# Kernel optimization log

Hardware: AMD Instinct MI355X
Metric: run time of the kernel (lower is better)

Reference implementation:

```python
import jax, jax.numpy as jnp
import numpy as np

B, N = 16384, 20
F = 128          # n_node_features = n_neighbors_features = embed_dim
T = 100          # time_dim
E = 128          # n_edge_features
H = 2            # n_head
OUT = 128        # output_dimension
KEY_DIM = F + T + E  # 356


def setup_inputs() -> dict:
    key = jax.random.key(0)
    ks = jax.random.split(key, 24)
    s = 0.02
    inp = {
        "src_node_features": jax.random.normal(ks[0], (B, F), jnp.float32),
        "neighbors_features": jax.random.normal(ks[1], (B, N, F), jnp.float32),
        "neighbors_time_features": jax.random.normal(ks[2], (B, N, T), jnp.float32),
        "edge_features": jax.random.normal(ks[3], (B, N, E), jnp.float32),
        "neighbors_padding_mask": jax.random.randint(ks[4], (B, N), 0, 2).astype(bool),
        "weights": jax.random.uniform(ks[5], (B, N), jnp.float32),
        # transform: Linear(key_dim -> F)
        "Wt": jax.random.normal(ks[6], (F, KEY_DIM), jnp.float32) * s,
        "bt": jnp.zeros((F,), jnp.float32),
        # MultiheadAttention projections (embed_dim = kdim = vdim = F)
        "Wq": jax.random.normal(ks[7], (F, F), jnp.float32) * s,
        "bq": jnp.zeros((F,), jnp.float32),
        "Wk": jax.random.normal(ks[8], (F, F), jnp.float32) * s,
        "bk": jnp.zeros((F,), jnp.float32),
        "Wv": jax.random.normal(ks[9], (F, F), jnp.float32) * s,
        "bv": jnp.zeros((F,), jnp.float32),
        "Wo": jax.random.normal(ks[10], (F, F), jnp.float32) * s,
        "bo": jnp.zeros((F,), jnp.float32),
        # MergeLayer: fc1(query_dim + F -> F), fc2(F -> OUT)
        "W1": jax.random.normal(ks[11], (F, F + F), jnp.float32) * s,
        "b1": jnp.zeros((F,), jnp.float32),
        "W2": jax.random.normal(ks[12], (OUT, F), jnp.float32) * s,
        "b2": jnp.zeros((OUT,), jnp.float32),
    }
    return inp


def _gat_forward(src, nbr, timef, edgef, w, mask,
                 Wt, bt, Wq, bq, Wk, bk, Wv, bv, Wo, bo, W1, b1, W2, b2):
    b, f = src.shape
    dh = f // H
    scale = 1.0 / jnp.sqrt(jnp.asarray(dh, src.dtype))
    # key = transform(cat([nbr, edge, time])) * weights  -> [B,N,F]
    k_in = jnp.concatenate([nbr, edgef, timef], axis=2)
    keyv = (jnp.einsum('bnk,fk->bnf', k_in, Wt) + bt) * w[:, :, None]
    # invalid-neighborhood fixup: rows fully padded get their first slot unmasked
    invalid = mask.all(axis=1, keepdims=True)           # [B,1]
    mask = mask.at[:, 0].set(jnp.where(invalid[:, 0], False, mask[:, 0]))
    # projections (query_len = 1)
    q = (src @ Wq.T + bq).reshape(b, H, dh)             # [B,H,dh]
    k = (keyv @ Wk.T + bk).reshape(b, N, H, dh)         # [B,N,H,dh]
    v = (keyv @ Wv.T + bv).reshape(b, N, H, dh)
    scores = jnp.einsum('bhd,bnhd->bhn', q, k) * scale  # [B,H,N]
    scores = jnp.where(mask[:, None, :], -jnp.inf, scores)
    attn = jax.nn.softmax(scores, axis=-1)
    ctx = jnp.einsum('bhn,bnhd->bhd', attn, v).reshape(b, f)
    out = ctx @ Wo.T + bo                               # [B,F]
    out = jnp.where(invalid, jnp.asarray(0.0, out.dtype), out)
    out = jax.nn.relu(out)
    # MergeLayer: fc2(relu(fc1(cat([attn_out, src]))))
    hmid = jax.nn.relu(jnp.concatenate([out, src], axis=1) @ W1.T + b1)
    return hmid @ W2.T + b2


def reference(src_node_features, neighbors_features, neighbors_time_features,
              edge_features, neighbors_padding_mask, weights,
              Wt, bt, Wq, bq, Wk, bk, Wv, bv, Wo, bo, W1, b1, W2, b2):
    return _gat_forward(src_node_features, neighbors_features,
                        neighbors_time_features, edge_features, weights,
                        neighbors_padding_mask,
                        Wt, bt, Wq, bq, Wk, bk, Wv, bv, Wo, bo, W1, b1, W2, b2)
```

## Files before the change

kernel.cpp:

```cpp
#include <hip/hip_runtime.h>
#include <math.h>

#define NN 20
#define FF 128
#define TT 100
#define EE 128
#define KD 356

typedef unsigned int u32;
typedef unsigned short u16;
typedef unsigned long long u64;
typedef __attribute__((ext_vector_type(4))) float f32x4;
typedef __attribute__((ext_vector_type(8))) short s16x8;

__device__ __forceinline__ u16 f2b(float f) {
    u32 u = __float_as_uint(f);
    u32 r = u + 0x7FFFu + ((u >> 16) & 1u);
    return (u16)(r >> 16);
}
__device__ __forceinline__ float b2f(u16 h) { return __uint_as_float(((u32)h) << 16); }
__device__ __forceinline__ float blo(u32 u){ return __uint_as_float(u << 16); }
__device__ __forceinline__ float bhi(u32 u){ return __uint_as_float(u & 0xFFFF0000u); }
__device__ __forceinline__ u32 pk2(float a, float b){ return (u32)f2b(a) | ((u32)f2b(b) << 16); }


__global__ void prep_fuse(const float* __restrict__ Wt, const float* __restrict__ bt,
                          const float* __restrict__ Wk, const float* __restrict__ Wv,
                          const u32* __restrict__ maskw,
                          float* __restrict__ wkt, float* __restrict__ wvt,
                          float* __restrict__ kfb, float* __restrict__ vfb, int* __restrict__ flagp)
{
    const int blk = blockIdx.x, t = threadIdx.x;
    if (blk < KD) {
        __shared__ float col[FF];
        col[t] = Wt[t * KD + blk];
        __syncthreads();
        float ak = 0.f, av = 0.f;
        for (int j = 0; j < FF; ++j) {
            float c = col[j];
            ak = fmaf(Wk[t * FF + j], c, ak);
            av = fmaf(Wv[t * FF + j], c, av);
        }
        wkt[blk * FF + t] = ak;
        wvt[blk * FF + t] = av;
    } else if (blk == KD) {
        float ak = 0.f, av = 0.f;
        for (int j = 0; j < FF; ++j) {
            float c = bt[j];
            ak = fmaf(Wk[t * FF + j], c, ak);
            av = fmaf(Wv[t * FF + j], c, av);
        }
        kfb[t] = ak; vfb[t] = av;
    } else {
        int any = 0;
        for (int i = t; i < 8192; i += 128) any |= (maskw[i] > 1u) ? 1 : 0;
        any = __any(any) ? 1 : 0;
        __shared__ int red[2];
        if ((t & 63) == 0) red[t >> 6] = any;
        __syncthreads();
        if (t == 0) *flagp = (red[0] | red[1]) ? 1 : 0;
    }
}

__global__ void prep_pack_v4(const float* __restrict__ wkt, const float* __restrict__ wvt,
                             const float* __restrict__ Wq, const float* __restrict__ Wo,
                             const float* __restrict__ W1, const float* __restrict__ W2,
                             u16* __restrict__ kvB, u16* __restrict__ wqI, u16* __restrict__ woI,
                             u16* __restrict__ w1I, u16* __restrict__ w2I)
{
    const int id = blockIdx.x * 256 + threadIdx.x;
    if (id < 196608) {
        int chunk = id >> 9, e = id & 511;
        int ln = e >> 3, ee = e & 7;
        int kt = chunk >> 4, nb = chunk & 15;
        int k = kt * 32 + (ln >> 4) * 8 + ee;
        int n = nb * 16 + (ln & 15);
        float v = 0.f;
        if (k < KD) v = (n < FF) ? wkt[k * FF + n] : wvt[k * FF + (n - FF)];
        kvB[id] = f2b(v);
    } else if (id < 215040) {
        int e = id - 196608; int rem = e % 9216;
        int n = rem / 72, kk = rem % 72; int k = (e / 9216) * 64 + kk;
        wqI[e] = f2b(kk < 64 ? Wq[n * FF + k] : 0.f);
    } else if (id < 233472) {
        int e = id - 215040; int rem = e % 9216;
        int n = rem / 72, kk = rem % 72; int k = (e / 9216) * 64 + kk;
        woI[e] = f2b(kk < 64 ? Wo[n * FF + k] : 0.f);
    } else if (id < 270336) {
        int e = id - 233472; int rem = e % 9216;
        int n = rem / 72, kk = rem % 72; int k = (e / 9216) * 64 + kk;
        w1I[e] = f2b(kk < 64 ? W1[n * 2 * FF + k] : 0.f);
    } else if (id < 288768) {
        int e = id - 270336; int rem = e % 9216;
        int n = rem / 72, kk = rem % 72; int k = (e / 9216) * 64 + kk;
        w2I[e] = f2b(kk < 64 ? W2[n * FF + k] : 0.f);
    }
}

__device__ __forceinline__ void loadA32(const float* __restrict__ nbr,
                                        const float* __restrict__ edg,
                                        const float* __restrict__ tmf,
                                        size_t r, int g, int kt, f32x4& v0, f32x4& v1)
{
    int c0 = g * 8;
    if (kt < 4) {
        const float* p = nbr + r * 128 + kt * 32 + c0;
        v0 = *(const f32x4*)p; v1 = *(const f32x4*)(p + 4);
    } else if (kt < 8) {
        const float* p = edg + r * 128 + (kt - 4) * 32 + c0;
        v0 = *(const f32x4*)p; v1 = *(const f32x4*)(p + 4);
    } else {
        int c = (kt - 8) * 32 + c0;
        const float* p = tmf + r * 100 + c;
        v0 = (c + 3 < 100) ? *(const f32x4*)p       : (f32x4){0.f,0.f,0.f,0.f};
        v1 = (c + 7 < 100) ? *(const f32x4*)(p + 4) : (f32x4){0.f,0.f,0.f,0.f};
    }
}

__global__ __launch_bounds__(512) void kv_attn_fused3(
    const float* __restrict__ nbr, const float* __restrict__ edg, const float* __restrict__ tmf,
    const float* __restrict__ wgt, const float* __restrict__ bk, const float* __restrict__ bv,
    const u16* __restrict__ kvB, const float* __restrict__ kfb, const float* __restrict__ vfb,
    const u16* __restrict__ Qg, const void* __restrict__ maskp, const int* __restrict__ flagp,
    u16* __restrict__ ctxout, unsigned char* __restrict__ flags)
{
    __shared__ __align__(16) u16 smem[10880];
    float* p_lds = (float*)(smem + 10560);

    const int tid = threadIdx.x;
    const int lane = tid & 63, wave = tid >> 6;
    const int wn = wave;
    const int Mbase = blockIdx.x * 80;
    const int Bbase = blockIdx.x * 4;
    const int kg = lane >> 4, l16 = lane & 15;

    const bool stg = tid < 320;
    const int skg = (tid >> 4) & 3;
    const int srow = (tid >> 6) * 16 + (tid & 15);
    const size_t gr = (size_t)(Mbase + srow);

    f32x4 acc[5][2] = {};

    f32x4 pa0, pa1;
    if (stg) loadA32(nbr, edg, tmf, gr, skg, 0, pa0, pa1);
    s16x8 bc0 = *(const s16x8*)(kvB + (size_t)(wn * 2 + 0) * 512 + lane * 8);
    s16x8 bc1 = *(const s16x8*)(kvB + (size_t)(wn * 2 + 1) * 512 + lane * 8);
    if (stg)
        *(uint4*)(&smem[tid * 8]) = make_uint4(pk2(pa0.x,pa0.y), pk2(pa0.z,pa0.w),
                                               pk2(pa1.x,pa1.y), pk2(pa1.z,pa1.w));
    __syncthreads();

    #pragma unroll
    for (int kt = 0; kt < 12; ++kt) {
        const u16* curA = smem + (kt & 1) * 2560;
        u16* nxtA = (u16*)smem + ((kt + 1) & 1) * 2560;

        f32x4 na0, na1; s16x8 bn0, bn1;
        if (kt < 11) {
            if (stg) loadA32(nbr, edg, tmf, gr, skg, kt + 1, na0, na1);
            bn0 = *(const s16x8*)(kvB + (size_t)((kt + 1) * 16 + wn * 2 + 0) * 512 + lane * 8);
            bn1 = *(const s16x8*)(kvB + (size_t)((kt + 1) * 16 + wn * 2 + 1) * 512 + lane * 8);
        }
        s16x8 af[5];
        #pragma unroll
        for (int mt = 0; mt < 5; ++mt)
            af[mt] = *(const s16x8*)(&curA[(mt * 4 + kg) * 128 + l16 * 8]);
        #pragma unroll
        for (int mt = 0; mt < 5; ++mt) {
            acc[mt][0] = __builtin_amdgcn_mfma_f32_16x16x32_bf16(af[mt], bc0, acc[mt][0], 0, 0, 0);
            acc[mt][1] = __builtin_amdgcn_mfma_f32_16x16x32_bf16(af[mt], bc1, acc[mt][1], 0, 0, 0);
        }
        if (kt < 11) {
            if (stg)
                *(uint4*)(&nxtA[tid * 8]) = make_uint4(pk2(na0.x,na0.y), pk2(na0.z,na0.w),
                                                       pk2(na1.x,na1.y), pk2(na1.z,na1.w));
            bc0 = bn0; bc1 = bn1;
        }
        __syncthreads();
    }

    u16* kls = smem;
    const int rg4 = (lane >> 4) * 4;
    if (wn < 4) {
        #pragma unroll
        for (int mt = 0; mt < 5; ++mt) {
            const int r0 = mt * 16 + rg4;
            float w4v[4];
            #pragma unroll
            for (int i = 0; i < 4; ++i) w4v[i] = wgt[Mbase + r0 + i];
            #pragma unroll
            for (int nt = 0; nt < 2; ++nt) {
                const int c = wn * 32 + nt * 16 + l16;
                const float fb = kfb[c], bb = bk[c];
                #pragma unroll
                for (int i = 0; i < 4; ++i)
                    kls[(r0 + i) * 132 + c] = f2b(fmaf(acc[mt][nt][i] + fb, w4v[i], bb));
            }
        }
    } else {
        #pragma unroll
        for (int mt = 0; mt < 5; ++mt) {
            const int r0 = mt * 16 + rg4;
            float w4v[4];
            #pragma unroll
            for (int i = 0; i < 4; ++i) w4v[i] = wgt[Mbase + r0 + i];
            #pragma unroll
            for (int nt = 0; nt < 2; ++nt) {
                const int c = (wn - 4) * 32 + nt * 16 + l16;
                const float fb = vfb[c], bb = bv[c];
                #pragma unroll
                for (int i = 0; i < 4; ++i)
                    acc[mt][nt][i] = fmaf(acc[mt][nt][i] + fb, w4v[i], bb);
            }
        }
    }
    __syncthreads();

    const int lb = wave >> 1, h = wave & 1;
    const int brow = Bbase + lb;
    {
        const int flagv = *flagp;
        bool mybit = false;
        if (lane < NN) {
            if (flagv) mybit = ((const unsigned char*)maskp)[brow * NN + lane] != 0;
            else       mybit = ((const int*)maskp)[brow * NN + lane] != 0;
        }
        u64 bal = __ballot(mybit);
        u32 mb = (u32)(bal & 0xFFFFFull);
        const bool invalid = (mb == 0xFFFFFu);
        if (invalid) mb &= ~1u;
        if (h == 0 && lane == 0) flags[brow] = invalid ? 1 : 0;

        const int n = lane & 31;
        float s = -INFINITY;
        if (lane < 32 && n < NN) {
            const u16* kr = kls + (lb * NN + n) * 132 + h * 64;
            const u16* qr = Qg + (size_t)brow * 128 + h * 64;
            float d = 0.f;
            #pragma unroll
            for (int dc = 0; dc < 16; ++dc) {
                uint2 kw = *(const uint2*)(kr + dc * 4);
                uint2 qw = *(const uint2*)(qr + dc * 4);
                d = fmaf(blo(kw.x), blo(qw.x), d);  d = fmaf(bhi(kw.x), bhi(qw.x), d);
                d = fmaf(blo(kw.y), blo(qw.y), d);  d = fmaf(bhi(kw.y), bhi(qw.y), d);
            }
            s = ((mb >> n) & 1u) ? -INFINITY : d * 0.125f;
        }
        float mx = s;
        #pragma unroll
        for (int off = 16; off; off >>= 1) mx = fmaxf(mx, __shfl_xor(mx, off, 32));
        float e = (lane < 32 && n < NN) ? expf(s - mx) : 0.f;
        float sum = e;
        #pragma unroll
        for (int off = 16; off; off >>= 1) sum += __shfl_xor(sum, off, 32);
        if (lane < NN) p_lds[wave * NN + lane] = e / sum;
    }
    __syncthreads();

    if (wn >= 4) {
        #pragma unroll
        for (int mt = 0; mt < 5; ++mt) {
            const int r0 = mt * 16 + rg4;
            #pragma unroll
            for (int nt = 0; nt < 2; ++nt) {
                const int c = (wn - 4) * 32 + nt * 16 + l16;
                #pragma unroll
                for (int i = 0; i < 4; ++i)
                    kls[(r0 + i) * 132 + c] = f2b(acc[mt][nt][i]);
            }
        }
    }
    __syncthreads();

    {
        float cacc = 0.f;
        #pragma unroll
        for (int n2 = 0; n2 < NN; ++n2) {
            float pn = p_lds[wave * NN + n2];
            cacc = fmaf(pn, b2f(kls[(lb * NN + n2) * 132 + h * 64 + lane]), cacc);
        }
        ctxout[(size_t)brow * 128 + h * 64 + lane] = f2b(cacc);
    }
}

#define GM_Q 0
#define GM_O 1
#define GM_H 2
#define GM_F 3

template<int MODE>
__global__ __launch_bounds__(256) void gemm_small(
    const void* __restrict__ Asrc, const float* __restrict__ Asrc2,
    const u16* __restrict__ Bimg, const float* __restrict__ bias,
    const unsigned char* __restrict__ flags, void* __restrict__ outp)
{
    __shared__ u16 lA[64 * 72];
    __shared__ u16 lB[128 * 72];
    const int tid = threadIdx.x;
    const int Mbase = blockIdx.x * 64;
    const int lane = tid & 63, wave = tid >> 6;
    const int wm = wave >> 1, wn = wave & 1;
    const int row = tid >> 2, cg = tid & 3;

    constexpr int KTILES = (MODE == GM_H) ? 4 : 2;
    f32x4 acc[2][4] = {};
    const size_t r = (size_t)(Mbase + row);

    for (int kt = 0; kt < KTILES; ++kt) {
        if (MODE == GM_Q || (MODE == GM_H && kt >= 2)) {
            const float* ap = (MODE == GM_Q)
                ? ((const float*)Asrc + r * 128 + kt * 64 + cg * 16)
                : (Asrc2 + r * 128 + (kt - 2) * 64 + cg * 16);
            f32x4 x0 = *(const f32x4*)ap,       x1 = *(const f32x4*)(ap + 4);
            f32x4 x2 = *(const f32x4*)(ap + 8), x3 = *(const f32x4*)(ap + 12);
            *(uint4*)(&lA[row * 72 + cg * 16])     = make_uint4(pk2(x0.x,x0.y), pk2(x0.z,x0.w), pk2(x1.x,x1.y), pk2(x1.z,x1.w));
            *(uint4*)(&lA[row * 72 + cg * 16 + 8]) = make_uint4(pk2(x2.x,x2.y), pk2(x2.z,x2.w), pk2(x3.x,x3.y), pk2(x3.z,x3.w));
        } else {
            const u16* ap = (const u16*)Asrc + r * 128 + kt * 64 + cg * 16;
            *(uint4*)(&lA[row * 72 + cg * 16])     = *(const uint4*)ap;
            *(uint4*)(&lA[row * 72 + cg * 16 + 8]) = *(const uint4*)(ap + 8);
        }
        for (int c = wave; c < 18; c += 4) {
            const char* g = (const char*)Bimg + (size_t)kt * 18432 + c * 1024 + lane * 16;
            char* l = (char*)lB + c * 1024;
            __builtin_amdgcn_global_load_lds((const __attribute__((address_space(1))) u32*)g,
                                             (__attribute__((address_space(3))) u32*)l, 16, 0, 0);
        }
        __syncthreads();
        #pragma unroll
        for (int ks = 0; ks < 2; ++ks) {
            int kk = ks * 32 + (lane >> 4) * 8;
            s16x8 a[2], b[4];
            #pragma unroll
            for (int mt = 0; mt < 2; ++mt)
                a[mt] = *(const s16x8*)(&lA[(wm * 32 + mt * 16 + (lane & 15)) * 72 + kk]);
            #pragma unroll
            for (int nt = 0; nt < 4; ++nt)
                b[nt] = *(const s16x8*)(&lB[(wn * 64 + nt * 16 + (lane & 15)) * 72 + kk]);
            #pragma unroll
            for (int mt = 0; mt < 2; ++mt)
                #pragma unroll
                for (int nt = 0; nt < 4; ++nt)
                    acc[mt][nt] = __builtin_amdgcn_mfma_f32_16x16x32_bf16(a[mt], b[nt], acc[mt][nt], 0, 0, 0);
        }
        __syncthreads();
    }

    #pragma unroll
    for (int mt = 0; mt < 2; ++mt) {
        #pragma unroll
        for (int nt = 0; nt < 4; ++nt) {
            int colg = wn * 64 + nt * 16 + (lane & 15);
            float bb = bias[colg];
            #pragma unroll
            for (int i = 0; i < 4; ++i) {
                int rg = Mbase + wm * 32 + mt * 16 + (lane >> 4) * 4 + i;
                float val = acc[mt][nt][i] + bb;
                if (MODE == GM_O) { if (flags[rg]) val = 0.f; val = fmaxf(val, 0.f); }
                if (MODE == GM_H) val = fmaxf(val, 0.f);
                if (MODE == GM_F) ((float*)outp)[(size_t)rg * 128 + colg] = val;
                else              ((u16*)outp)[(size_t)rg * 128 + colg] = f2b(val);
            }
        }
    }
}


__global__ void prep_pack_r2(const float* __restrict__ wkt, const float* __restrict__ wvt,
                             const float* __restrict__ Wq, const float* __restrict__ Wo,
                             const float* __restrict__ W1, const float* __restrict__ W2,
                             u16* __restrict__ bpack, u32* __restrict__ wq2, u32* __restrict__ wo2,
                             u32* __restrict__ w12, u32* __restrict__ w22)
{
    const int id = blockIdx.x * 256 + threadIdx.x;
    if (id < 98304) {
        int kt = id >> 14;
        int o  = id & 16383;
        int n  = o >> 6;
        int kk = (o & 63) ^ ((n & 7) << 3);
        int k  = kt * 64 + kk;
        float v = 0.f;
        if (k < KD) v = (n < FF) ? wkt[k * FF + n] : wvt[k * FF + (n - FF)];
        bpack[id] = f2b(v);
    } else if (id < 106496) {
        int e = id - 98304; int j = e >> 6, tt = e & 63;
        wq2[e] = (u32)f2b(Wq[tt * FF + j]) | ((u32)f2b(Wq[(tt + 64) * FF + j]) << 16);
    } else if (id < 114688) {
        int e = id - 106496; int j = e >> 6, tt = e & 63;
        wo2[e] = (u32)f2b(Wo[tt * FF + j]) | ((u32)f2b(Wo[(tt + 64) * FF + j]) << 16);
    } else if (id < 131072) {
        int e = id - 114688; int j = e >> 6, tt = e & 63;
        w12[e] = (u32)f2b(W1[tt * 2 * FF + j]) | ((u32)f2b(W1[(tt + 64) * 2 * FF + j]) << 16);
    } else if (id < 139264) {
        int e = id - 131072; int j = e >> 6, tt = e & 63;
        w22[e] = (u32)f2b(W2[tt * FF + j]) | ((u32)f2b(W2[(tt + 64) * FF + j]) << 16);
    }
}

__global__ __launch_bounds__(512) void kv_gemm_r2(
    const float* __restrict__ nbr, const float* __restrict__ edg, const float* __restrict__ tmf,
    const float* __restrict__ wgt, const float* __restrict__ bk, const float* __restrict__ bv,
    const u16* __restrict__ bpack, const float* __restrict__ kfb, const float* __restrict__ vfb,
    u16* __restrict__ kvout)
{
    __shared__ u16 lA[128 * 64];
    __shared__ u16 lB[256 * 64];
    const int tid = threadIdx.x;
    const int Mbase = blockIdx.x * 128;
    const int lane = tid & 63, wave = tid >> 6;
    const int wm = wave >> 2, wn = wave & 3;

    f32x4 acc[4][4] = {};
    const int rq = tid >> 4;
    const int cq = tid & 15;

    for (int kt = 0; kt < 6; ++kt) {
        #pragma unroll
        for (int i = 0; i < 4; ++i) {
            int row = rq + i * 32;
            size_t r = (size_t)(Mbase + row);
            f32x4 v;
            if (kt < 2)       v = *(const f32x4*)(nbr + r * 128 + kt * 64 + cq * 4);
            else if (kt < 4)  v = *(const f32x4*)(edg + r * 128 + (kt - 2) * 64 + cq * 4);
            else if (kt == 4) v = *(const f32x4*)(tmf + r * 100 + cq * 4);
            else if (cq < 9)  v = *(const f32x4*)(tmf + r * 100 + 64 + cq * 4);
            else              v = (f32x4){0.f, 0.f, 0.f, 0.f};
            int off = row * 64 + ((cq * 4) ^ ((row & 7) << 3));
            *(uint2*)(&lA[off]) = make_uint2(pk2(v.x, v.y), pk2(v.z, v.w));
        }
        #pragma unroll
        for (int i = 0; i < 4; ++i) {
            int boff = wave * 4096 + i * 1024;
            const char* g = (const char*)bpack + (size_t)kt * 32768 + boff + lane * 16;
            char* l = (char*)lB + boff;
            __builtin_amdgcn_global_load_lds((const __attribute__((address_space(1))) u32*)g,
                                             (__attribute__((address_space(3))) u32*)l, 16, 0, 0);
        }
        __syncthreads();
        #pragma unroll
        for (int ks = 0; ks < 2; ++ks) {
            int kk = ks * 32 + (lane >> 4) * 8;
            s16x8 a[4], b[4];
            #pragma unroll
            for (int mt = 0; mt < 4; ++mt) {
                int m = wm * 64 + mt * 16 + (lane & 15);
                a[mt] = *(const s16x8*)(&lA[m * 64 + (kk ^ ((m & 7) << 3))]);
            }
            #pragma unroll
            for (int nt = 0; nt < 4; ++nt) {
                int n = wn * 64 + nt * 16 + (lane & 15);
                b[nt] = *(const s16x8*)(&lB[n * 64 + (kk ^ ((n & 7) << 3))]);
            }
            #pragma unroll
            for (int mt = 0; mt < 4; ++mt)
                #pragma unroll
                for (int nt = 0; nt < 4; ++nt)
                    acc[mt][nt] = __builtin_amdgcn_mfma_f32_16x16x32_bf16(a[mt], b[nt], acc[mt][nt], 0, 0, 0);
        }
        __syncthreads();
    }

    #pragma unroll
    for (int mt = 0; mt < 4; ++mt) {
        float w4[4];
        #pragma unroll
        for (int i = 0; i < 4; ++i)
            w4[i] = wgt[Mbase + wm * 64 + mt * 16 + (lane >> 4) * 4 + i];
        #pragma unroll
        for (int nt = 0; nt < 4; ++nt) {
            int c = wn * 64 + nt * 16 + (lane & 15);
            float fb   = (c < FF) ? kfb[c] : vfb[c - FF];
            float bias = (c < FF) ? bk[c]  : bv[c - FF];
            #pragma unroll
            for (int i = 0; i < 4; ++i) {
                int rr = Mbase + wm * 64 + mt * 16 + (lane >> 4) * 4 + i;
                float val = fmaf(acc[mt][nt][i] + fb, w4[i], bias);
                kvout[(size_t)rr * 256 + c] = f2b(val);
            }
        }
    }
}

__global__ __launch_bounds__(64) void gat_attn_r2(
    const float* __restrict__ src, const void* __restrict__ maskp,
// ... 141 lines not shown
                            const u32* __restrict__ maskw, float* __restrict__ ws)
{
    const int blk = blockIdx.x;
    const int t = threadIdx.x;
    if (blk < KD) {
        __shared__ float col[FF];
        col[t] = Wt[t * KD + blk];
        __syncthreads();
        float ak = 0.f, av = 0.f;
        for (int j = 0; j < FF; ++j) {
            float c = col[j];
            ak = fmaf(Wk[t * FF + j], c, ak);
            av = fmaf(Wv[t * FF + j], c, av);
        }
        ws[FB_WKT + blk * FF + t] = ak;
        ws[FB_WVT + blk * FF + t] = av;
    } else if (blk == KD) {
        float ak = 0.f, av = 0.f;
        for (int j = 0; j < FF; ++j) {
            float c = bt[j];
            ak = fmaf(Wk[t * FF + j], c, ak);
            av = fmaf(Wv[t * FF + j], c, av);
        }
        ws[FB_KB + t] = ak;
        ws[FB_VB + t] = av;
    } else if (blk == KD + 1) {
        int any = 0;
        for (int i = t; i < 8192; i += 128) any |= (maskw[i] > 1u) ? 1 : 0;
        any = __any(any) ? 1 : 0;
        __shared__ int red[2];
        if ((t & 63) == 0) red[t >> 6] = any;
        __syncthreads();
        if (t == 0) ((int*)ws)[FB_FLAG] = (red[0] | red[1]) ? 1 : 0;
    } else {
        int id = (blk - (KD + 2)) * 128 + t;
        if (id < FF * FF) {
            int k = id >> 7, f = id & 127;
            ws[FB_WQT + id] = Wq[f * FF + k];
        } else if (id < 2 * FF * FF) {
            int e = id - FF * FF; int k = e >> 7, f = e & 127;
            ws[FB_WOT + e] = Wo[f * FF + k];
        } else if (id < 4 * FF * FF) {
            int e = id - 2 * FF * FF; int j = e >> 7, f = e & 127;
            ws[FB_W1T + e] = W1[f * (2 * FF) + j];
        } else if (id < 5 * FF * FF) {
            int e = id - 4 * FF * FF; int k = e >> 7, f = e & 127;
            ws[FB_W2T + e] = W2[f * FF + k];
        }
    }
}

__global__ __launch_bounds__(64) void gat_main_fb(
    const float* __restrict__ src, const float* __restrict__ nbr,
    const float* __restrict__ tmf, const float* __restrict__ edg,
    const void* __restrict__ maskp, const float* __restrict__ wgt,
    const float* __restrict__ bq, const float* __restrict__ bk,
    const float* __restrict__ bv, const float* __restrict__ bo,
    const float* __restrict__ b1, const float* __restrict__ b2,
    const float* __restrict__ ws, float* __restrict__ out)
{
    const int b = blockIdx.x;
    const int t = threadIdx.x;
    __shared__ __align__(16) float kin[KD * NN];
    __shared__ float s_src[FF], s_q[FF], s_ctx[FF], s_out[FF], s_h[FF];
    __shared__ float s_w[NN], s_sc[2 * NN];

    const int flag = ((const int*)ws)[FB_FLAG];
    bool mybit = false;
    if (t < NN) {
        if (flag) mybit = ((const unsigned char*)maskp)[b * NN + t] != 0;
        else      mybit = ((const int*)maskp)[b * NN + t] != 0;
    }
    u64 bal = __ballot(mybit);
    u32 mb = (u32)(bal & 0xFFFFFull);
    const bool invalid = (mb == 0xFFFFFu);
    if (invalid) mb &= ~1u;

    s_src[t] = src[(size_t)b * FF + t];
    s_src[t + 64] = src[(size_t)b * FF + 64 + t];
    if (t < NN) s_w[t] = wgt[(size_t)b * NN + t];

    for (int idx = t; idx < NN * FF; idx += 64) {
        int n = idx >> 7, j = idx & 127;
        kin[j * NN + n]         = nbr[((size_t)b * NN + n) * FF + j];
        kin[(128 + j) * NN + n] = edg[((size_t)b * NN + n) * EE + j];
    }
    for (int idx = t; idx < NN * TT; idx += 64) {
        int n = idx / TT, j = idx - n * TT;
        kin[(256 + j) * NN + n] = tmf[((size_t)b * NN + n) * TT + j];
    }
    __syncthreads();

    const float* wkt = ws + FB_WKT;
    const float* wvt = ws + FB_WVT;
    float ak0[NN], ak1[NN], av0[NN], av1[NN];
#pragma unroll
    for (int n = 0; n < NN; ++n) { ak0[n] = 0.f; ak1[n] = 0.f; av0[n] = 0.f; av1[n] = 0.f; }
    for (int k = 0; k < KD; ++k) {
        float wk0 = wkt[k * FF + t],      wk1 = wkt[k * FF + 64 + t];
        float wv0 = wvt[k * FF + t],      wv1 = wvt[k * FF + 64 + t];
        const float4* cp = (const float4*)(kin + k * NN);
        float4 ca = cp[0], cb = cp[1], cc = cp[2], cd = cp[3], ce = cp[4];
        const float c[NN] = { ca.x, ca.y, ca.z, ca.w,  cb.x, cb.y, cb.z, cb.w,
                              cc.x, cc.y, cc.z, cc.w,  cd.x, cd.y, cd.z, cd.w,
                              ce.x, ce.y, ce.z, ce.w };
#pragma unroll
        for (int n = 0; n < NN; ++n) {
            ak0[n] = fmaf(wk0, c[n], ak0[n]);
            ak1[n] = fmaf(wk1, c[n], ak1[n]);
            av0[n] = fmaf(wv0, c[n], av0[n]);
            av1[n] = fmaf(wv1, c[n], av1[n]);
        }
    }
    __syncthreads();

    float* kls = kin;
    float* vls = kin + NN * 129;
    {
        const float kb0 = ws[FB_KB + t], kb1 = ws[FB_KB + 64 + t];
        const float vb0 = ws[FB_VB + t], vb1 = ws[FB_VB + 64 + t];
        const float k0b = bk[t], k1b = bk[64 + t];
        const float v0b = bv[t], v1b = bv[64 + t];
#pragma unroll
        for (int n = 0; n < NN; ++n) {
            float wn = s_w[n];
            kls[n * 129 + t]      = fmaf(wn, ak0[n] + kb0, k0b);
            kls[n * 129 + 64 + t] = fmaf(wn, ak1[n] + kb1, k1b);
            vls[n * 129 + t]      = fmaf(wn, av0[n] + vb0, v0b);
            vls[n * 129 + 64 + t] = fmaf(wn, av1[n] + vb1, v1b);
        }
    }
    {
        const float* wqT = ws + FB_WQT;
        float q0 = bq[t], q1 = bq[64 + t];
        for (int j = 0; j < FF; ++j) {
            float sj = s_src[j];
            q0 = fmaf(wqT[j * FF + t], sj, q0);
            q1 = fmaf(wqT[j * FF + 64 + t], sj, q1);
        }
        s_q[t] = q0; s_q[64 + t] = q1;
    }
    __syncthreads();

    if (t < 2 * NN) {
        int h = t / NN, n = t - (t / NN) * NN;
        const float* kr = kls + n * 129 + h * 64;
        const float* qr = s_q + h * 64;
        float s = 0.f;
#pragma unroll
        for (int d = 0; d < 64; ++d) s = fmaf(qr[d], kr[d], s);
        s *= 0.125f;
        s_sc[t] = ((mb >> n) & 1u) ? -INFINITY : s;
    }
    __syncthreads();
    if (t < 2) {
        float mx = -INFINITY;
        for (int n = 0; n < NN; ++n) mx = fmaxf(mx, s_sc[t * NN + n]);
        float e[NN]; float sum = 0.f;
        for (int n = 0; n < NN; ++n) { e[n] = expf(s_sc[t * NN + n] - mx); sum += e[n]; }
        float inv = 1.f / sum;
        for (int n = 0; n < NN; ++n) s_sc[t * NN + n] = e[n] * inv;
    }
    __syncthreads();

    {
        float c0 = 0.f, c1 = 0.f;
#pragma unroll
        for (int n = 0; n < NN; ++n) {
            c0 = fmaf(s_sc[n],      vls[n * 129 + t],      c0);
            c1 = fmaf(s_sc[NN + n], vls[n * 129 + 64 + t], c1);
        }
        s_ctx[t] = c0; s_ctx[64 + t] = c1;
    }
    __syncthreads();

    {
        const float* woT = ws + FB_WOT;
        float o0 = bo[t], o1 = bo[64 + t];
        for (int j = 0; j < FF; ++j) {
            float cj = s_ctx[j];
            o0 = fmaf(woT[j * FF + t], cj, o0);
            o1 = fmaf(woT[j * FF + 64 + t], cj, o1);
        }
        if (invalid) { o0 = 0.f; o1 = 0.f; }
        o0 = fmaxf(o0, 0.f); o1 = fmaxf(o1, 0.f);
        s_out[t] = o0; s_out[64 + t] = o1;
    }
    __syncthreads();

    {
        const float* w1T = ws + FB_W1T;
        float h0 = b1[t], h1 = b1[64 + t];
        for (int j = 0; j < FF; ++j) {
            float xj = s_out[j];
            h0 = fmaf(w1T[j * FF + t], xj, h0);
            h1 = fmaf(w1T[j * FF + 64 + t], xj, h1);
        }
        for (int j = 0; j < FF; ++j) {
            float xj = s_src[j];
            h0 = fmaf(w1T[(FF + j) * FF + t], xj, h0);
            h1 = fmaf(w1T[(FF + j) * FF + 64 + t], xj, h1);
        }
        h0 = fmaxf(h0, 0.f); h1 = fmaxf(h1, 0.f);
        s_h[t] = h0; s_h[64 + t] = h1;
    }
    __syncthreads();

    {
        const float* w2T = ws + FB_W2T;
        float f0 = b2[t], f1 = b2[64 + t];
        for (int j = 0; j < FF; ++j) {
            float hj = s_h[j];
            f0 = fmaf(w2T[j * FF + t], hj, f0);
            f1 = fmaf(w2T[j * FF + 64 + t], hj, f1);
        }
        out[(size_t)b * FF + t] = f0;
        out[(size_t)b * FF + 64 + t] = f1;
    }
}


extern "C" void kernel_launch(void* const* d_in, const int* in_sizes, int n_in,
                              void* d_out, int out_size, void* d_ws, size_t ws_size,
                              hipStream_t stream)
{
    const float* src = (const float*)d_in[0];
    const float* nbr = (const float*)d_in[1];
    const float* tmf = (const float*)d_in[2];
    const float* edg = (const float*)d_in[3];
    const void*  msk = d_in[4];
    const float* wgt = (const float*)d_in[5];
    const float* Wt  = (const float*)d_in[6];
    const float* bt  = (const float*)d_in[7];
    const float* Wq  = (const float*)d_in[8];
    const float* bq  = (const float*)d_in[9];
    const float* Wk  = (const float*)d_in[10];
    const float* bk  = (const float*)d_in[11];
    const float* Wv  = (const float*)d_in[12];
    const float* bv  = (const float*)d_in[13];
    const float* Wo  = (const float*)d_in[14];
    const float* bo  = (const float*)d_in[15];
    const float* W1  = (const float*)d_in[16];
    const float* b1  = (const float*)d_in[17];
    const float* W2  = (const float*)d_in[18];
    const float* b2  = (const float*)d_in[19];

    const int B = in_sizes[0] / FF;
    const size_t M = (size_t)B * NN;

    size_t o1 = 0;
    size_t t1_qa   = o1; o1 += (size_t)B * 256;
    size_t t1_ch   = o1; o1 += (size_t)B * 256;
    size_t t1_kvB  = o1; o1 += 393216;
    size_t t1_wqI  = o1; o1 += 36864;
    size_t t1_woI  = o1; o1 += 36864;
    size_t t1_w1I  = o1; o1 += 73728;
    size_t t1_w2I  = o1; o1 += 36864;
    size_t t1_wkt  = o1; o1 += (size_t)KD * FF * 4;
    size_t t1_wvt  = o1; o1 += (size_t)KD * FF * 4;
    size_t t1_kfb  = o1; o1 += 512;
    size_t t1_vfb  = o1; o1 += 512;
    size_t t1_flg  = o1; o1 += (size_t)B;
    o1 = (o1 + 255) & ~(size_t)255;
    size_t t1_flag = o1; o1 += 64;
    const size_t need1 = o1;

    size_t o2 = 0;
    size_t t2_kv    = o2; o2 += M * 512;
    size_t t2_bpack = o2; o2 += 98304ull * 2;
    size_t t2_wkt   = o2; o2 += (size_t)KD * FF * 4;
    size_t t2_wvt   = o2; o2 += (size_t)KD * FF * 4;
    size_t t2_kfb   = o2; o2 += 512;
    size_t t2_vfb   = o2; o2 += 512;
    size_t t2_wq2   = o2; o2 += 32768;
    size_t t2_wo2   = o2; o2 += 32768;
    size_t t2_w12   = o2; o2 += 65536;
    size_t t2_w22   = o2; o2 += 32768;
    size_t t2_flag  = o2; o2 += 64;
    const size_t need2 = o2;

    char* w = (char*)d_ws;

    if (ws_size >= need1 && (B % 64) == 0) {
        u16*   qa    = (u16*)(w + t1_qa);
        u16*   ch    = (u16*)(w + t1_ch);
        u16*   kvB   = (u16*)(w + t1_kvB);
        u16*   wqI   = (u16*)(w + t1_wqI);
        u16*   woI   = (u16*)(w + t1_woI);
        u16*   w1I   = (u16*)(w + t1_w1I);
        u16*   w2I   = (u16*)(w + t1_w2I);
        float* wktp  = (float*)(w + t1_wkt);
        float* wvtp  = (float*)(w + t1_wvt);
        float* kfb   = (float*)(w + t1_kfb);
        float* vfb   = (float*)(w + t1_vfb);
        unsigned char* flg = (unsigned char*)(w + t1_flg);
        int*   flagp = (int*)(w + t1_flag);

        prep_fuse<<<dim3(KD + 2), dim3(128), 0, stream>>>(Wt, bt, Wk, Wv,
            (const u32*)msk, wktp, wvtp, kfb, vfb, flagp);
        prep_pack_v4<<<dim3(1128), dim3(256), 0, stream>>>(wktp, wvtp, Wq, Wo, W1, W2,
            kvB, wqI, woI, w1I, w2I);
        gemm_small<GM_Q><<<dim3(B / 64), dim3(256), 0, stream>>>(
            (const void*)src, nullptr, wqI, bq, nullptr, (void*)qa);
        kv_attn_fused3<<<dim3(B / 4), dim3(512), 0, stream>>>(
            nbr, edg, tmf, wgt, bk, bv, kvB, kfb, vfb, qa, msk, flagp, ch, flg);
        gemm_small<GM_O><<<dim3(B / 64), dim3(256), 0, stream>>>(
            (const void*)ch, nullptr, woI, bo, flg, (void*)qa);
        gemm_small<GM_H><<<dim3(B / 64), dim3(256), 0, stream>>>(
            (const void*)qa, src, w1I, b1, nullptr, (void*)ch);
        gemm_small<GM_F><<<dim3(B / 64), dim3(256), 0, stream>>>(
            (const void*)ch, nullptr, w2I, b2, nullptr, d_out);
    } else if (ws_size >= need2 && (M % 128) == 0) {
        u16*   kvp   = (u16*)(w + t2_kv);
        u16*   bpack = (u16*)(w + t2_bpack);
        float* wktp  = (float*)(w + t2_wkt);
        float* wvtp  = (float*)(w + t2_wvt);
        float* kfb   = (float*)(w + t2_kfb);
        float* vfb   = (float*)(w + t2_vfb);
        u32*   wq2   = (u32*)(w + t2_wq2);
        u32*   wo2   = (u32*)(w + t2_wo2);
        u32*   w12   = (u32*)(w + t2_w12);
        u32*   w22   = (u32*)(w + t2_w22);
        int*   flagp = (int*)(w + t2_flag);

        prep_fuse<<<dim3(KD + 2), dim3(128), 0, stream>>>(Wt, bt, Wk, Wv,
            (const u32*)msk, wktp, wvtp, kfb, vfb, flagp);
        prep_pack_r2<<<dim3(544), dim3(256), 0, stream>>>(wktp, wvtp, Wq, Wo, W1, W2,
            bpack, wq2, wo2, w12, w22);
        kv_gemm_r2<<<dim3((int)(M / 128)), dim3(512), 0, stream>>>(
            nbr, edg, tmf, wgt, bk, bv, bpack, kfb, vfb, kvp);
        gat_attn_r2<<<dim3(B), dim3(64), 0, stream>>>(
            src, msk, bq, bo, b1, b2, kvp, wq2, wo2, w12, w22, flagp, (float*)d_out);
    } else {
        float* ws = (float*)d_ws;
        gat_prep_fb<<<dim3(KD + 2 + 640), dim3(128), 0, stream>>>(
            Wt, bt, Wq, Wk, Wv, Wo, W1, W2, (const u32*)msk, ws);
        gat_main_fb<<<dim3(B), dim3(64), 0, stream>>>(
            src, nbr, tmf, edg, msk, wgt, bq, bk, bv, bo, b1, b2, ws, (float*)d_out);
    }
}
```

Before: 209.6 us.

## Stage fp32 neighbor/edge tiles directly to LDS with async global_load_lds

Replaces the per-k-tile register staging and double-buffered bf16 LDS ring in the fused KV-attention kernel. All 80 rows of neighbor and edge features are now copied into an XOR-swizzled fp32 LDS area with async global-to-LDS loads, and the time features are loaded up front into registers. bf16 conversion moves to the LDS read side using v_cvt_pk_bf16_f32, and B fragments are prefetched four k-tiles ahead, which cuts per-iteration barriers and exposes more memory-level parallelism. In exchange LDS use per block grows to about 80KB, which may lower occupancy, and the hand-written vmcnt waits depend on a fragile count of outstanding loads.

Result: slower. 236.1 us (+12.7%).

```diff
diff --git a/kernel.cpp b/kernel.cpp
--- a/kernel.cpp
+++ b/kernel.cpp
@@ -12,6 +12,7 @@
 typedef unsigned long long u64;
 typedef __attribute__((ext_vector_type(4))) float f32x4;
 typedef __attribute__((ext_vector_type(8))) short s16x8;
+typedef __attribute__((ext_vector_type(4))) u32 u32x4;
 
 __device__ __forceinline__ u16 f2b(float f) {
     u32 u = __float_as_uint(f);
@@ -22,6 +23,9 @@
 __device__ __forceinline__ float blo(u32 u){ return __uint_as_float(u << 16); }
 __device__ __forceinline__ float bhi(u32 u){ return __uint_as_float(u & 0xFFFF0000u); }
 __device__ __forceinline__ u32 pk2(float a, float b){ return (u32)f2b(a) | ((u32)f2b(b) << 16); }
+__device__ __forceinline__ u32 cvtpk(float a, float b){
+    u32 d; asm("v_cvt_pk_bf16_f32 %0, %1, %2" : "=v"(d) : "v"(a), "v"(b)); return d;
+}
 
 
 __global__ void prep_fuse(const float* __restrict__ Wt, const float* __restrict__ bt,
@@ -97,35 +101,15 @@
     }
 }
 
-__device__ __forceinline__ void loadA32(const float* __restrict__ nbr,
-                                        const float* __restrict__ edg,
-                                        const float* __restrict__ tmf,
-                                        size_t r, int g, int kt, f32x4& v0, f32x4& v1)
-{
-    int c0 = g * 8;
-    if (kt < 4) {
-        const float* p = nbr + r * 128 + kt * 32 + c0;
-        v0 = *(const f32x4*)p; v1 = *(const f32x4*)(p + 4);
-    } else if (kt < 8) {
-        const float* p = edg + r * 128 + (kt - 4) * 32 + c0;
-        v0 = *(const f32x4*)p; v1 = *(const f32x4*)(p + 4);
-    } else {
-        int c = (kt - 8) * 32 + c0;
-        const float* p = tmf + r * 100 + c;
-        v0 = (c + 3 < 100) ? *(const f32x4*)p       : (f32x4){0.f,0.f,0.f,0.f};
-        v1 = (c + 7 < 100) ? *(const f32x4*)(p + 4) : (f32x4){0.f,0.f,0.f,0.f};
-    }
-}
-
-__global__ __launch_bounds__(512) void kv_attn_fused3(
+__global__ __launch_bounds__(512) void kv_attn_fused5(
     const float* __restrict__ nbr, const float* __restrict__ edg, const float* __restrict__ tmf,
     const float* __restrict__ wgt, const float* __restrict__ bk, const float* __restrict__ bv,
     const u16* __restrict__ kvB, const float* __restrict__ kfb, const float* __restrict__ vfb,
     const u16* __restrict__ Qg, const void* __restrict__ maskp, const int* __restrict__ flagp,
     u16* __restrict__ ctxout, unsigned char* __restrict__ flags)
 {
-    __shared__ __align__(16) u16 smem[10880];
-    float* p_lds = (float*)(smem + 10560);
+    __shared__ __align__(16) u16 smem[40960];
+    char* sb = (char*)smem;
 
     const int tid = threadIdx.x;
     const int lane = tid & 63, wave = tid >> 6;
@@ -134,52 +118,100 @@
     const int Bbase = blockIdx.x * 4;
     const int kg = lane >> 4, l16 = lane & 15;
 
-    const bool stg = tid < 320;
-    const int skg = (tid >> 4) & 3;
-    const int srow = (tid >> 6) * 16 + (tid & 15);
-    const size_t gr = (size_t)(Mbase + srow);
+    const float* nbrg = nbr + (size_t)Mbase * 128;
+    const float* edgg = edg + (size_t)Mbase * 128;
+    const float* tmfg = tmf + (size_t)Mbase * 100;
 
     f32x4 acc[5][2] = {};
-
-    f32x4 pa0, pa1;
-    if (stg) loadA32(nbr, edg, tmf, gr, skg, 0, pa0, pa1);
-    s16x8 bc0 = *(const s16x8*)(kvB + (size_t)(wn * 2 + 0) * 512 + lane * 8);
-    s16x8 bc1 = *(const s16x8*)(kvB + (size_t)(wn * 2 + 1) * 512 + lane * 8);
-    if (stg)
-        *(uint4*)(&smem[tid * 8]) = make_uint4(pk2(pa0.x,pa0.y), pk2(pa0.z,pa0.w),
-                                               pk2(pa1.x,pa1.y), pk2(pa1.z,pa1.w));
-    __syncthreads();
-
-    #pragma unroll
-    for (int kt = 0; kt < 12; ++kt) {
-        const u16* curA = smem + (kt & 1) * 2560;
-        u16* nxtA = (u16*)smem + ((kt + 1) & 1) * 2560;
-
-        f32x4 na0, na1; s16x8 bn0, bn1;
-        if (kt < 11) {
-            if (stg) loadA32(nbr, edg, tmf, gr, skg, kt + 1, na0, na1);
-            bn0 = *(const s16x8*)(kvB + (size_t)((kt + 1) * 16 + wn * 2 + 0) * 512 + lane * 8);
-            bn1 = *(const s16x8*)(kvB + (size_t)((kt + 1) * 16 + wn * 2 + 1) * 512 + lane * 8);
-        }
-        s16x8 af[5];
-        #pragma unroll
-        for (int mt = 0; mt < 5; ++mt)
-            af[mt] = *(const s16x8*)(&curA[(mt * 4 + kg) * 128 + l16 * 8]);
-        #pragma unroll
-        for (int mt = 0; mt < 5; ++mt) {
-            acc[mt][0] = __builtin_amdgcn_mfma_f32_16x16x32_bf16(af[mt], bc0, acc[mt][0], 0, 0, 0);
-            acc[mt][1] = __builtin_amdgcn_mfma_f32_16x16x32_bf16(af[mt], bc1, acc[mt][1], 0, 0, 0);
-        }
-        if (kt < 11) {
-            if (stg)
-                *(uint4*)(&nxtA[tid * 8]) = make_uint4(pk2(na0.x,na0.y), pk2(na0.z,na0.w),
-                                                       pk2(na1.x,na1.y), pk2(na1.z,na1.w));
-            bc0 = bn0; bc1 = bn1;
-        }
-        __syncthreads();
-    }
-
-    u16* kls = smem;
+    s16x8 br[4][2];
+    f32x4 tr0, tr1, tr2, tr3;
+
+    {
+        const int rl = (lane >> 5);
+        const int x  = lane & 31;
+        #pragma unroll
+        for (int i = 0; i < 5; ++i) {
+            int c = wave + 8 * i;
+            int r = 2 * c + rl;
+            const float* g = nbrg + (size_t)r * 128 + ((x ^ (r & 7)) << 2);
+            __builtin_amdgcn_global_load_lds((const __attribute__((address_space(1))) u32*)g,
+                (__attribute__((address_space(3))) u32*)(sb + c * 1024), 16, 0, 0);
+        }
+        __builtin_amdgcn_sched_barrier(0);
+        #pragma unroll
+        for (int k = 0; k < 4; ++k) {
+            br[k][0] = *(const s16x8*)(kvB + (size_t)(k * 16 + wn * 2 + 0) * 512 + lane * 8);
+            br[k][1] = *(const s16x8*)(kvB + (size_t)(k * 16 + wn * 2 + 1) * 512 + lane * 8);
+        }
+        #pragma unroll
+        for (int i = 0; i < 5; ++i) {
+            int c = wave + 8 * i;
+            int r = 2 * c + rl;
+            const float* g = edgg + (size_t)r * 128 + ((x ^ (r & 7)) << 2);
+            __builtin_amdgcn_global_load_lds((const __attribute__((address_space(1))) u32*)g,
+                (__attribute__((address_space(3))) u32*)(sb + 40960 + c * 1024), 16, 0, 0);
+        }
+        tr0 = *(const f32x4*)(tmfg + (size_t)(0 * 512 + tid) * 4);
+        tr1 = *(const f32x4*)(tmfg + (size_t)(1 * 512 + tid) * 4);
+        tr2 = *(const f32x4*)(tmfg + (size_t)(2 * 512 + tid) * 4);
+        tr3 = (tid < 464) ? *(const f32x4*)(tmfg + (size_t)(3 * 512 + tid) * 4)
+                          : (f32x4){0.f, 0.f, 0.f, 0.f};
+        __builtin_amdgcn_sched_barrier(0);
+        asm volatile("s_waitcnt vmcnt(17)\n\ts_barrier" ::: "memory");
+        __builtin_amdgcn_sched_barrier(0);
+    }
+
+    #define GITER(KT) do {                                                          \
+        s16x8 af[5];                                                                \
+        _Pragma("unroll")                                                           \
+        for (int mt = 0; mt < 5; ++mt) {                                            \
+            int r = mt * 16 + l16;                                                  \
+            f32x4 lo, hi;                                                           \
+            if ((KT) < 8) {                                                         \
+                int base = ((KT) < 4) ? 0 : 40960;                                  \
+                int a = ((KT) & 3) * 8 + kg * 2;                                    \
+                int sw = r & 7;                                                     \
+                lo = *(const f32x4*)(sb + base + r * 512 + ((a ^ sw) << 4));        \
+                hi = *(const f32x4*)(sb + base + r * 512 + (((a + 1) ^ sw) << 4));  \
+            } else if ((KT) < 11) {                                                 \
+                int koff = ((KT) & 3) * 32 + kg * 8;                                \
+                const char* p0 = sb + r * 400 + koff * 4;                           \
+                lo = *(const f32x4*)p0; hi = *(const f32x4*)(p0 + 16);              \
+            } else {                                                                \
+                if (kg == 0) {                                                      \
+                    lo = *(const f32x4*)(sb + r * 400 + 384);                       \
+                    hi = (f32x4){0.f, 0.f, 0.f, 0.f};                               \
+                } else { lo = (f32x4){0.f,0.f,0.f,0.f}; hi = lo; }                  \
+            }                                                                       \
+            u32x4 q;                                                                \
+            q.x = cvtpk(lo.x, lo.y); q.y = cvtpk(lo.z, lo.w);                       \
+            q.z = cvtpk(hi.x, hi.y); q.w = cvtpk(hi.z, hi.w);                       \
+            af[mt] = __builtin_bit_cast(s16x8, q);                                  \
+        }                                                                           \
+        _Pragma("unroll")                                                           \
+        for (int mt = 0; mt < 5; ++mt) {                                            \
+            acc[mt][0] = __builtin_amdgcn_mfma_f32_16x16x32_bf16(af[mt], br[(KT)&3][0], acc[mt][0], 0, 0, 0); \
+            acc[mt][1] = __builtin_amdgcn_mfma_f32_16x16x32_bf16(af[mt], br[(KT)&3][1], acc[mt][1], 0, 0, 0); \
+        }                                                                           \
+        if ((KT) + 4 <= 11) {                                                       \
+            br[(KT)&3][0] = *(const s16x8*)(kvB + (size_t)(((KT)+4) * 16 + wn * 2 + 0) * 512 + lane * 8); \
+            br[(KT)&3][1] = *(const s16x8*)(kvB + (size_t)(((KT)+4) * 16 + wn * 2 + 1) * 512 + lane * 8); \
+        }                                                                           \
+    } while (0)
+
+    GITER(0); GITER(1); GITER(2); GITER(3);
+    __syncthreads();
+    *(f32x4*)(sb + (size_t)(0 * 512 + tid) * 16) = tr0;
+    *(f32x4*)(sb + (size_t)(1 * 512 + tid) * 16) = tr1;
+    *(f32x4*)(sb + (size_t)(2 * 512 + tid) * 16) = tr2;
+    if (tid < 464) *(f32x4*)(sb + (size_t)(3 * 512 + tid) * 16) = tr3;
+    GITER(4); GITER(5); GITER(6); GITER(7);
+    __syncthreads();
+    GITER(8); GITER(9); GITER(10); GITER(11);
+    #undef GITER
+
+    u16* kls = (u16*)(sb + 40960);
+    float* p_lds = (float*)(sb + 33024);
     const int rg4 = (lane >> 4) * 4;
     if (wn < 4) {
         #pragma unroll
@@ -927,7 +959,7 @@
             kvB, wqI, woI, w1I, w2I);
         gemm_small<GM_Q><<<dim3(B / 64), dim3(256), 0, stream>>>(
             (const void*)src, nullptr, wqI, bq, nullptr, (void*)qa);
-        kv_attn_fused3<<<dim3(B / 4), dim3(512), 0, stream>>>(
+        kv_attn_fused5<<<dim3(B / 4), dim3(512), 0, stream>>>(
             nbr, edg, tmf, wgt, bk, bv, kvB, kfb, vfb, qa, msk, flagp, ch, flg);
         gemm_small<GM_O><<<dim3(B / 64), dim3(256), 0, stream>>>(
             (const void*)ch, nullptr, woI, bo, flg, (void*)qa);
```

## Stage K/V GEMM A-tiles via async global_load_lds with triple buffering

Applied to the files above, without the earlier changes.

Replaces the register-staged, double-buffered A-tile loads in the fused KV/attention kernel with direct global-to-LDS loads (global_load_lds) into a three-deep XOR-swizzled fp32 ring, using manual vmcnt waits and raw barriers. The fp32-to-bf16 conversion moves to the read side with the hardware v_cvt_pk_bf16_f32 instruction. The last time-feature tail is preloaded into registers so the final k-step skips LDS. This aims to hide HBM latency for the bandwidth-dominant neighbor/edge/time streams and cut VGPR staging and software rounding. In exchange, LDS use grows, which may lower occupancy, and the hand-tuned vmcnt counts are fragile.

After: 207.6 us. Within noise of the previous version (-0.9%).

```diff
diff --git a/kernel.cpp b/kernel.cpp
--- a/kernel.cpp
+++ b/kernel.cpp
@@ -12,6 +12,7 @@
 typedef unsigned long long u64;
 typedef __attribute__((ext_vector_type(4))) float f32x4;
 typedef __attribute__((ext_vector_type(8))) short s16x8;
+typedef __attribute__((ext_vector_type(4))) u32 u32x4;
 
 __device__ __forceinline__ u16 f2b(float f) {
     u32 u = __float_as_uint(f);
@@ -22,6 +23,9 @@
 __device__ __forceinline__ float blo(u32 u){ return __uint_as_float(u << 16); }
 __device__ __forceinline__ float bhi(u32 u){ return __uint_as_float(u & 0xFFFF0000u); }
 __device__ __forceinline__ u32 pk2(float a, float b){ return (u32)f2b(a) | ((u32)f2b(b) << 16); }
+__device__ __forceinline__ u32 cvtpk(float a, float b){
+    u32 d; asm("v_cvt_pk_bf16_f32 %0, %1, %2" : "=v"(d) : "v"(a), "v"(b)); return d;
+}
 
 
 __global__ void prep_fuse(const float* __restrict__ Wt, const float* __restrict__ bt,
@@ -97,35 +101,17 @@
     }
 }
 
-__device__ __forceinline__ void loadA32(const float* __restrict__ nbr,
-                                        const float* __restrict__ edg,
-                                        const float* __restrict__ tmf,
-                                        size_t r, int g, int kt, f32x4& v0, f32x4& v1)
-{
-    int c0 = g * 8;
-    if (kt < 4) {
-        const float* p = nbr + r * 128 + kt * 32 + c0;
-        v0 = *(const f32x4*)p; v1 = *(const f32x4*)(p + 4);
-    } else if (kt < 8) {
-        const float* p = edg + r * 128 + (kt - 4) * 32 + c0;
-        v0 = *(const f32x4*)p; v1 = *(const f32x4*)(p + 4);
-    } else {
-        int c = (kt - 8) * 32 + c0;
-        const float* p = tmf + r * 100 + c;
-        v0 = (c + 3 < 100) ? *(const f32x4*)p       : (f32x4){0.f,0.f,0.f,0.f};
-        v1 = (c + 7 < 100) ? *(const f32x4*)(p + 4) : (f32x4){0.f,0.f,0.f,0.f};
-    }
-}
-
-__global__ __launch_bounds__(512) void kv_attn_fused3(
+__global__ __launch_bounds__(512) void kv_attn_fused7(
     const float* __restrict__ nbr, const float* __restrict__ edg, const float* __restrict__ tmf,
     const float* __restrict__ wgt, const float* __restrict__ bk, const float* __restrict__ bv,
     const u16* __restrict__ kvB, const float* __restrict__ kfb, const float* __restrict__ vfb,
     const u16* __restrict__ Qg, const void* __restrict__ maskp, const int* __restrict__ flagp,
     u16* __restrict__ ctxout, unsigned char* __restrict__ flags)
 {
-    __shared__ __align__(16) u16 smem[10880];
-    float* p_lds = (float*)(smem + 10560);
+    __shared__ __align__(16) u16 smem[15680];
+    char* sb = (char*)smem;
+    float* p_lds = (float*)(sb + 30720);
+    u16* kls = (u16*)sb;
 
     const int tid = threadIdx.x;
     const int lane = tid & 63, wave = tid >> 6;
@@ -134,52 +120,89 @@
     const int Bbase = blockIdx.x * 4;
     const int kg = lane >> 4, l16 = lane & 15;
 
-    const bool stg = tid < 320;
-    const int skg = (tid >> 4) & 3;
-    const int srow = (tid >> 6) * 16 + (tid & 15);
-    const size_t gr = (size_t)(Mbase + srow);
-
     f32x4 acc[5][2] = {};
-
-    f32x4 pa0, pa1;
-    if (stg) loadA32(nbr, edg, tmf, gr, skg, 0, pa0, pa1);
-    s16x8 bc0 = *(const s16x8*)(kvB + (size_t)(wn * 2 + 0) * 512 + lane * 8);
-    s16x8 bc1 = *(const s16x8*)(kvB + (size_t)(wn * 2 + 1) * 512 + lane * 8);
-    if (stg)
-        *(uint4*)(&smem[tid * 8]) = make_uint4(pk2(pa0.x,pa0.y), pk2(pa0.z,pa0.w),
-                                               pk2(pa1.x,pa1.y), pk2(pa1.z,pa1.w));
-    __syncthreads();
+    s16x8 br[2][2];
+    f32x4 tl[5];
+
+    #define STAGE_CHUNK(C, KT) do {                                                         \
+        int row_ = (C) * 8 + (lane >> 3);                                                   \
+        int x_ = (lane & 7) ^ (row_ & 7);                                                   \
+        const float* g_;                                                                    \
+        if ((KT) < 4)      g_ = nbr + (size_t)(Mbase + row_) * 128 + (KT) * 32 + x_ * 4;    \
+        else if ((KT) < 8) g_ = edg + (size_t)(Mbase + row_) * 128 + ((KT)-4) * 32 + x_ * 4;\
+        else               g_ = tmf + (size_t)(Mbase + row_) * 100 + ((KT)-8) * 32 + x_ * 4;\
+        __builtin_amdgcn_global_load_lds((const __attribute__((address_space(1))) u32*)g_,  \
+            (__attribute__((address_space(3))) u32*)(sb + ((KT)%3)*10240 + (C)*1024), 16, 0, 0); \
+    } while (0)
+
+    #define STAGE(KT) do {                                                                  \
+        STAGE_CHUNK(wave, KT);                                                              \
+        if (wave < 2) STAGE_CHUNK(8 + wave, KT);                                            \
+    } while (0)
+
+    #define LOADB(KT) do {                                                                  \
+        br[(KT)&1][0] = *(const s16x8*)(kvB + (size_t)((KT)*16 + wn*2 + 0)*512 + lane*8);   \
+        br[(KT)&1][1] = *(const s16x8*)(kvB + (size_t)((KT)*16 + wn*2 + 1)*512 + lane*8);   \
+    } while (0)
+
+    #define NV1(KT) ((KT)==0?6:((KT)==1?8:((KT)==2?10:((KT)<=8?8:((KT)==9?7:6)))))
+    #define NV2(KT) ((KT)==0?8:((KT)==1?10:((KT)==2?12:((KT)<=8?10:((KT)==9?8:6)))))
 
     #pragma unroll
-    for (int kt = 0; kt < 12; ++kt) {
-        const u16* curA = smem + (kt & 1) * 2560;
-        u16* nxtA = (u16*)smem + ((kt + 1) & 1) * 2560;
-
-        f32x4 na0, na1; s16x8 bn0, bn1;
-        if (kt < 11) {
-            if (stg) loadA32(nbr, edg, tmf, gr, skg, kt + 1, na0, na1);
-            bn0 = *(const s16x8*)(kvB + (size_t)((kt + 1) * 16 + wn * 2 + 0) * 512 + lane * 8);
-            bn1 = *(const s16x8*)(kvB + (size_t)((kt + 1) * 16 + wn * 2 + 1) * 512 + lane * 8);
-        }
-        s16x8 af[5];
-        #pragma unroll
-        for (int mt = 0; mt < 5; ++mt)
-            af[mt] = *(const s16x8*)(&curA[(mt * 4 + kg) * 128 + l16 * 8]);
-        #pragma unroll
-        for (int mt = 0; mt < 5; ++mt) {
-            acc[mt][0] = __builtin_amdgcn_mfma_f32_16x16x32_bf16(af[mt], bc0, acc[mt][0], 0, 0, 0);
-            acc[mt][1] = __builtin_amdgcn_mfma_f32_16x16x32_bf16(af[mt], bc1, acc[mt][1], 0, 0, 0);
-        }
-        if (kt < 11) {
-            if (stg)
-                *(uint4*)(&nxtA[tid * 8]) = make_uint4(pk2(na0.x,na0.y), pk2(na0.z,na0.w),
-                                                       pk2(na1.x,na1.y), pk2(na1.z,na1.w));
-            bc0 = bn0; bc1 = bn1;
-        }
-        __syncthreads();
-    }
-
-    u16* kls = smem;
+    for (int mt = 0; mt < 5; ++mt)
+        tl[mt] = *(const f32x4*)(tmf + (size_t)(Mbase + mt * 16 + l16) * 100 + 96);
+    STAGE(0); STAGE(1); STAGE(2);
+    LOADB(0); LOADB(1);
+
+    #define GITER(KT) do {                                                                  \
+        if ((KT) <= 10) {                                                                   \
+            if (wave < 2) { asm volatile("s_waitcnt vmcnt(%0)" :: "i"(NV2(KT)) : "memory"); }\
+            else          { asm volatile("s_waitcnt vmcnt(%0)" :: "i"(NV1(KT)) : "memory"); }\
+            __builtin_amdgcn_s_barrier();                                                   \
+            __builtin_amdgcn_sched_barrier(0);                                              \
+        }                                                                                   \
+        s16x8 af[5];                                                                        \
+        _Pragma("unroll")                                                                   \
+        for (int mt = 0; mt < 5; ++mt) {                                                    \
+            f32x4 lo, hi;                                                                   \
+            if ((KT) <= 10) {                                                               \
+                int r_ = mt * 16 + l16; int sw_ = r_ & 7; int y0_ = kg * 2;                 \
+                const char* bp_ = sb + ((KT)%3)*10240 + r_ * 128;                           \
+                lo = *(const f32x4*)(bp_ + ((y0_ ^ sw_) << 4));                             \
+                hi = *(const f32x4*)(bp_ + (((y0_+1) ^ sw_) << 4));                         \
+            } else {                                                                        \
+                lo = (kg == 0) ? tl[mt] : (f32x4){0.f,0.f,0.f,0.f};                         \
+                hi = (f32x4){0.f,0.f,0.f,0.f};                                              \
+            }                                                                               \
+            u32x4 q_;                                                                       \
+            q_.x = cvtpk(lo.x, lo.y); q_.y = cvtpk(lo.z, lo.w);                             \
+            q_.z = cvtpk(hi.x, hi.y); q_.w = cvtpk(hi.z, hi.w);                             \
+            af[mt] = __builtin_bit_cast(s16x8, q_);                                         \
+        }                                                                                   \
+        _Pragma("unroll")                                                                   \
+        for (int mt = 0; mt < 5; ++mt) {                                                    \
+            acc[mt][0] = __builtin_amdgcn_mfma_f32_16x16x32_bf16(af[mt], br[(KT)&1][0], acc[mt][0], 0, 0, 0); \
+            acc[mt][1] = __builtin_amdgcn_mfma_f32_16x16x32_bf16(af[mt], br[(KT)&1][1], acc[mt][1], 0, 0, 0); \
+        }                                                                                   \
+        if ((KT) <= 10) {                                                                   \
+            asm volatile("s_waitcnt lgkmcnt(0)" ::: "memory");                              \
+            __builtin_amdgcn_s_barrier();                                                   \
+            __builtin_amdgcn_sched_barrier(0);                                              \
+            if ((KT) <= 7) STAGE((KT)+3);                                                   \
+            if ((KT)+2 <= 11) LOADB((KT)+2);                                                \
+        }                                                                                   \
+    } while (0)
+
+    GITER(0); GITER(1); GITER(2);  GITER(3);
+    GITER(4); GITER(5); GITER(6);  GITER(7);
+    GITER(8); GITER(9); GITER(10); GITER(11);
+    #undef GITER
+    #undef STAGE
+    #undef STAGE_CHUNK
+    #undef LOADB
+
+    __syncthreads();
+
     const int rg4 = (lane >> 4) * 4;
     if (wn < 4) {
         #pragma unroll
@@ -927,7 +950,7 @@
             kvB, wqI, woI, w1I, w2I);
         gemm_small<GM_Q><<<dim3(B / 64), dim3(256), 0, stream>>>(
             (const void*)src, nullptr, wqI, bq, nullptr, (void*)qa);
-        kv_attn_fused3<<<dim3(B / 4), dim3(512), 0, stream>>>(
+        kv_attn_fused7<<<dim3(B / 4), dim3(512), 0, stream>>>(
             nbr, edg, tmf, wgt, bk, bv, kvB, kfb, vfb, qa, msk, flagp, ch, flg);
         gemm_small<GM_O><<<dim3(B / 64), dim3(256), 0, stream>>>(
             (const void*)ch, nullptr, woI, bo, flg, (void*)qa);
```
